# Performance work log

Hardware: AMD Instinct MI355X
Metric: run time of the kernel (lower is better)

Reference implementation:

```python
import jax, jax.numpy as jnp
import numpy as np

B, N, NC = 4, 1024, 512
D, NH, DK, DC = 768, 12, 64, 256
DF = 4 * D
EPS = 1e-5


def _ln(x, g, b):
    m = x.mean(-1, keepdims=True)
    v = ((x - m) ** 2).mean(-1, keepdims=True)
    return (x - m) * jax.lax.rsqrt(v + EPS) * g + b


def setup_inputs() -> dict:
    key = jax.random.key(0)
    ks = jax.random.split(key, 16)
    s = 0.02
    return {
        "x": jax.random.normal(ks[0], (B, N, D), jnp.float32),
        "hdse_bias": jax.random.normal(ks[1], (B, NH, N, N), jnp.float32),
        "context": jax.random.normal(ks[2], (B, NC, DC), jnp.float32),
        "node_mask": jnp.ones((B, N), bool),
        "context_mask": jnp.ones((B, NC), bool),
        "ln_sa_g": jnp.ones((D,), jnp.float32),
        "ln_sa_b": jnp.zeros((D,), jnp.float32),
        "w_qkv": jax.random.normal(ks[3], (D, 3 * D), jnp.float32) * s,
        "b_qkv": jnp.zeros((3 * D,), jnp.float32),
        "w_osa": jax.random.normal(ks[4], (D, D), jnp.float32) * s,
        "b_osa": jnp.zeros((D,), jnp.float32),
        "ln_ca_g": jnp.ones((D,), jnp.float32),
        "ln_ca_b": jnp.zeros((D,), jnp.float32),
        "w_q": jax.random.normal(ks[5], (D, D), jnp.float32) * s,
        "b_q": jnp.zeros((D,), jnp.float32),
        "w_kv": jax.random.normal(ks[6], (DC, 2 * D), jnp.float32) * s,
        "b_kv": jnp.zeros((2 * D,), jnp.float32),
        "w_oca": jax.random.normal(ks[7], (D, D), jnp.float32) * s,
        "b_oca": jnp.zeros((D,), jnp.float32),
        "ln_ff_g": jnp.ones((D,), jnp.float32),
        "ln_ff_b": jnp.zeros((D,), jnp.float32),
        "w_ff1": jax.random.normal(ks[8], (D, DF), jnp.float32) * s,
        "b_ff1": jnp.zeros((DF,), jnp.float32),
        "w_ff2": jax.random.normal(ks[9], (DF, D), jnp.float32) * s,
        "b_ff2": jnp.zeros((D,), jnp.float32),
    }


def reference(x, hdse_bias, context, node_mask, context_mask,
              ln_sa_g, ln_sa_b, w_qkv, b_qkv, w_osa, b_osa,
              ln_ca_g, ln_ca_b, w_q, b_q, w_kv, b_kv, w_oca, b_oca,
              ln_ff_g, ln_ff_b, w_ff1, b_ff1, w_ff2, b_ff2):
    scale = 1.0 / np.sqrt(DK).astype(np.float32)

    # ---- self-attention with HDSE bias ----
    h = _ln(x, ln_sa_g, ln_sa_b)
    qkv = (h @ w_qkv + b_qkv).reshape(B, N, 3, NH, DK)
    q = qkv[:, :, 0].transpose(0, 2, 1, 3)  # (B,NH,N,DK)
    k = qkv[:, :, 1].transpose(0, 2, 1, 3)
    v = qkv[:, :, 2].transpose(0, 2, 1, 3)
    scores = jnp.einsum('bhnd,bhmd->bhnm', q, k) * scale + hdse_bias
    scores = jnp.where(node_mask[:, None, None, :], scores, -1e9)
    attn = jax.nn.softmax(scores, axis=-1)
    sa = jnp.einsum('bhnm,bhmd->bhnd', attn, v).transpose(0, 2, 1, 3).reshape(B, N, D)
    x = x + sa @ w_osa + b_osa

    # ---- cross-attention to context ----
    h = _ln(x, ln_ca_g, ln_ca_b)
    qc = (h @ w_q + b_q).reshape(B, N, NH, DK).transpose(0, 2, 1, 3)
    kvc = (context @ w_kv + b_kv).reshape(B, NC, 2, NH, DK)
    kc = kvc[:, :, 0].transpose(0, 2, 1, 3)  # (B,NH,NC,DK)
    vc = kvc[:, :, 1].transpose(0, 2, 1, 3)
    sc = jnp.einsum('bhnd,bhmd->bhnm', qc, kc) * scale
    sc = jnp.where(context_mask[:, None, None, :], sc, -1e9)
    ca = jnp.einsum('bhnm,bhmd->bhnd', jax.nn.softmax(sc, axis=-1), vc)
    ca = ca.transpose(0, 2, 1, 3).reshape(B, N, D)
    x = x + ca @ w_oca + b_oca

    # ---- FFN (exact GELU, matching nn.GELU default) ----
    h = _ln(x, ln_ff_g, ln_ff_b)
    x = x + jax.nn.gelu(h @ w_ff1 + b_ff1, approximate=False) @ w_ff2 + b_ff2
    return x
```

## Files before the change

kernel.cpp:

```cpp
#include <hip/hip_runtime.h>
#include <hip/hip_bf16.h>
#include <math.h>
#include <stdint.h>

typedef __attribute__((ext_vector_type(8))) short bf16x8;
typedef __attribute__((ext_vector_type(4))) float f32x4;

#define NH_ 12

__global__ __launch_bounds__(256) void wtrans_kernel(const float* __restrict__ W,
    __hip_bfloat16* __restrict__ Wt, int K, int N)
{
  __shared__ float tile[32][33];
  int k0 = blockIdx.x * 32, n0 = blockIdx.y * 32;
  int tx = threadIdx.x & 31, ty = threadIdx.x >> 5;
#pragma unroll
  for (int i = 0; i < 4; i++) {
    int r = ty + i * 8;
    tile[r][tx] = W[(size_t)(k0 + r) * N + n0 + tx];
  }
  __syncthreads();
#pragma unroll
  for (int i = 0; i < 4; i++) {
    int r = ty + i * 8;
    Wt[(size_t)(n0 + r) * K + k0 + tx] = __float2bfloat16(tile[tx][r]);
  }
}

__global__ void cvt_kernel(const float* __restrict__ src, __hip_bfloat16* __restrict__ dst, int n)
{
  int i = blockIdx.x * 256 + threadIdx.x;
  if (i < n) dst[i] = __float2bfloat16(src[i]);
}

__global__ __launch_bounds__(256) void ln_kernel(const float* __restrict__ x,
    const float* __restrict__ gg, const float* __restrict__ bb,
    __hip_bfloat16* __restrict__ out)
{
  int row = blockIdx.x;
  int t = threadIdx.x;
  const float* xr = x + (size_t)row * 768;
  float v0 = xr[t], v1 = xr[t + 256], v2 = xr[t + 512];
  float s = v0 + v1 + v2;
  float s2 = v0 * v0 + v1 * v1 + v2 * v2;
  for (int o = 32; o; o >>= 1) { s += __shfl_down(s, o); s2 += __shfl_down(s2, o); }
  __shared__ float red[8];
  __shared__ float mv[2];
  int wid = t >> 6, lane = t & 63;
  if (lane == 0) { red[wid] = s; red[wid + 4] = s2; }
  __syncthreads();
  if (t == 0) {
    float S = red[0] + red[1] + red[2] + red[3];
    float S2 = red[4] + red[5] + red[6] + red[7];
    float mean = S * (1.0f / 768.0f);
    float var = S2 * (1.0f / 768.0f) - mean * mean;
    mv[0] = mean;
    mv[1] = rsqrtf(var + 1e-5f);
  }
  __syncthreads();
  float mean = mv[0], rstd = mv[1];
  __hip_bfloat16* orow = out + (size_t)row * 768;
  orow[t]       = __float2bfloat16((v0 - mean) * rstd * gg[t] + bb[t]);
  orow[t + 256] = __float2bfloat16((v1 - mean) * rstd * gg[t + 256] + bb[t + 256]);
  orow[t + 512] = __float2bfloat16((v2 - mean) * rstd * gg[t + 512] + bb[t + 512]);
}

__global__ void vtrans_kernel(const __hip_bfloat16* __restrict__ src,
    __hip_bfloat16* __restrict__ dst, int L, int srow, int soff)
{
  int idx = blockIdx.x * 256 + threadIdx.x;
  int n = idx & (L - 1);
  int rest = idx / L;
  int d = rest & 63;
  rest >>= 6;
  int h = rest % NH_;
  int b = rest / NH_;
  dst[idx] = src[(size_t)(b * L + n) * srow + soff + h * 64 + d];
}

template<int EPI>
__global__ __launch_bounds__(256) void gemm_bt(
    const __hip_bfloat16* A, const __hip_bfloat16* Bt,
    const float* __restrict__ bias, const float* resid,
    void* Cout, int M, int N, int K)
{
  __shared__ __align__(16) __hip_bfloat16 As[128 * 32];
  __shared__ __align__(16) __hip_bfloat16 Bs[128 * 32];
  const int tid = threadIdx.x;
  const int bm = blockIdx.y, bn = blockIdx.x;
  const int lane = tid & 63, wid = tid >> 6;
  const int wm = (wid >> 1) * 64, wn = (wid & 1) * 64;
  const int r = lane & 15, g = lane >> 4;
  const int arow = tid >> 2, acol = (tid & 3) * 8;
  f32x4 acc[4][4] = {};
  const __hip_bfloat16* Ag  = A  + (size_t)(bm * 128 + arow) * K + acol;
  const __hip_bfloat16* Ag2 = Ag + (size_t)64 * K;
  const __hip_bfloat16* Bg  = Bt + (size_t)(bn * 128 + arow) * K + acol;
  const __hip_bfloat16* Bg2 = Bg + (size_t)64 * K;
  for (int kt = 0; kt < K; kt += 32) {
    uint4 a0 = *(const uint4*)(Ag + kt);
    uint4 a1 = *(const uint4*)(Ag2 + kt);
    uint4 b0 = *(const uint4*)(Bg + kt);
    uint4 b1 = *(const uint4*)(Bg2 + kt);
    __syncthreads();
    *(uint4*)(As + arow * 32 + acol) = a0;
    *(uint4*)(As + (arow + 64) * 32 + acol) = a1;
    *(uint4*)(Bs + arow * 32 + acol) = b0;
    *(uint4*)(Bs + (arow + 64) * 32 + acol) = b1;
    __syncthreads();
    bf16x8 af[4], bfr[4];
#pragma unroll
    for (int i = 0; i < 4; i++) {
      af[i]  = *(const bf16x8*)(As + (wm + i * 16 + r) * 32 + g * 8);
      bfr[i] = *(const bf16x8*)(Bs + (wn + i * 16 + r) * 32 + g * 8);
    }
#pragma unroll
    for (int i = 0; i < 4; i++)
#pragma unroll
      for (int j = 0; j < 4; j++)
        acc[i][j] = __builtin_amdgcn_mfma_f32_16x16x32_bf16(af[i], bfr[j], acc[i][j], 0, 0, 0);
  }
#pragma unroll
  for (int i = 0; i < 4; i++)
#pragma unroll
    for (int j = 0; j < 4; j++)
#pragma unroll
      for (int q = 0; q < 4; q++) {
        int row = bm * 128 + wm + i * 16 + g * 4 + q;
        int col = bn * 128 + wn + j * 16 + r;
        float v = acc[i][j][q] + bias[col];
        if constexpr (EPI == 0) {
          ((__hip_bfloat16*)Cout)[(size_t)row * N + col] = __float2bfloat16(v);
        } else if constexpr (EPI == 1) {
          ((float*)Cout)[(size_t)row * N + col] = v + resid[(size_t)row * N + col];
        } else {
          float t = 0.5f * v * (1.0f + erff(v * 0.70710678118654752f));
          ((__hip_bfloat16*)Cout)[(size_t)row * N + col] = __float2bfloat16(t);
        }
      }
}

template<int L, bool HASBIAS>
__global__ __launch_bounds__(256) void attn_kernel(
    const __hip_bfloat16* Qp, int qstride,
    const __hip_bfloat16* Kp, int kstride,
    const __hip_bfloat16* Vt,
    const float* __restrict__ bias,
    __hip_bfloat16* Out, float scale)
{
  __shared__ __align__(16) __hip_bfloat16 qtile[16 * 64];
  __shared__ __align__(16) __hip_bfloat16 sP[16 * L];
  __shared__ float invs[16];
  const int qb = blockIdx.x, h = blockIdx.y, b = blockIdx.z;
  const int tid = threadIdx.x, lane = tid & 63, wid = tid >> 6;
  const int r = lane & 15, g = lane >> 4;
  {
    int row = tid >> 4, c4 = (tid & 15) * 4;
    const __hip_bfloat16* src = Qp + (size_t)(b * 1024 + qb * 16 + row) * qstride + h * 64 + c4;
    *(uint2*)(qtile + row * 64 + c4) = *(const uint2*)src;
  }
  __syncthreads();
  bf16x8 q0 = *(const bf16x8*)(qtile + r * 64 + g * 8);
  bf16x8 q1 = *(const bf16x8*)(qtile + r * 64 + 32 + g * 8);
  const int KB = L / 64;
#pragma unroll 4
  for (int kb = 0; kb < KB; kb++) {
    int key0 = wid * (L / 4) + kb * 16;
    const __hip_bfloat16* ks = Kp + (size_t)(b * L + key0 + r) * kstride + h * 64 + g * 8;
    bf16x8 k0 = *(const bf16x8*)ks;
    bf16x8 k1 = *(const bf16x8*)(ks + 32);
    f32x4 acc = {};
    acc = __builtin_amdgcn_mfma_f32_16x16x32_bf16(q0, k0, acc, 0, 0, 0);
    acc = __builtin_amdgcn_mfma_f32_16x16x32_bf16(q1, k1, acc, 0, 0, 0);
    int key = key0 + r;
#pragma unroll
    for (int q = 0; q < 4; q++) {
      int qrow = g * 4 + q;
      float s = acc[q] * scale;
      if constexpr (HASBIAS)
        s += bias[((size_t)(b * NH_ + h) * 1024 + qb * 16 + qrow) * L + key];
      sP[qrow * L + key] = __float2bfloat16(s);
    }
  }
  __syncthreads();
  {
    int row = tid >> 4, j0 = tid & 15;
    float m = -3.0e38f;
    for (int j = j0; j < L; j += 16) m = fmaxf(m, __bfloat162float(sP[row * L + j]));
#pragma unroll
    for (int o = 1; o < 16; o <<= 1) m = fmaxf(m, __shfl_xor(m, o));
    float sum = 0.0f;
    for (int j = j0; j < L; j += 16) {
      float p = expf(__bfloat162float(sP[row * L + j]) - m);
      sum += p;
      sP[row * L + j] = __float2bfloat16(p);
    }
#pragma unroll
    for (int o = 1; o < 16; o <<= 1) sum += __shfl_xor(sum, o);
    if (j0 == 0) invs[row] = 1.0f / sum;
  }
  __syncthreads();
  {
    int d0 = wid * 16;
    const __hip_bfloat16* vs = Vt + ((size_t)(b * NH_ + h) * 64 + d0 + r) * L + g * 8;
    f32x4 acc = {};
    for (int kb = 0; kb < L / 32; kb++) {
      bf16x8 pf = *(const bf16x8*)(sP + r * L + kb * 32 + g * 8);
      bf16x8 vf = *(const bf16x8*)(vs + kb * 32);
      acc = __builtin_amdgcn_mfma_f32_16x16x32_bf16(pf, vf, acc, 0, 0, 0);
    }
#pragma unroll
    for (int q = 0; q < 4; q++) {
      int qrow = g * 4 + q;
      float o = acc[q] * invs[qrow];
      Out[(size_t)(b * 1024 + qb * 16 + qrow) * 768 + h * 64 + d0 + r] = __float2bfloat16(o);
    }
  }
}

extern "C" void kernel_launch(void* const* d_in, const int* in_sizes, int n_in,
                              void* d_out, int out_size, void* d_ws, size_t ws_size,
                              hipStream_t stream)
{
  const float* x       = (const float*)d_in[0];
  const float* hdse    = (const float*)d_in[1];
  const float* ctx     = (const float*)d_in[2];
  const float* ln_sa_g = (const float*)d_in[5];
  const float* ln_sa_b = (const float*)d_in[6];
  const float* w_qkv   = (const float*)d_in[7];
  const float* b_qkv   = (const float*)d_in[8];
  const float* w_osa   = (const float*)d_in[9];
  const float* b_osa   = (const float*)d_in[10];
  const float* ln_ca_g = (const float*)d_in[11];
  const float* ln_ca_b = (const float*)d_in[12];
  const float* w_q     = (const float*)d_in[13];
  const float* b_q     = (const float*)d_in[14];
  const float* w_kv    = (const float*)d_in[15];
  const float* b_kv    = (const float*)d_in[16];
  const float* w_oca   = (const float*)d_in[17];
  const float* b_oca   = (const float*)d_in[18];
  const float* ln_ff_g = (const float*)d_in[19];
  const float* ln_ff_b = (const float*)d_in[20];
  const float* w_ff1   = (const float*)d_in[21];
  const float* b_ff1   = (const float*)d_in[22];
  const float* w_ff2   = (const float*)d_in[23];
  const float* b_ff2   = (const float*)d_in[24];

  char* ws = (char*)d_ws;
  __hip_bfloat16* wqkvT = (__hip_bfloat16*)(ws + 0);
  __hip_bfloat16* wosaT = (__hip_bfloat16*)(ws + 3538944);
  __hip_bfloat16* wqT   = (__hip_bfloat16*)(ws + 4718592);
  __hip_bfloat16* wkvT  = (__hip_bfloat16*)(ws + 5898240);
  __hip_bfloat16* wocaT = (__hip_bfloat16*)(ws + 6684672);
  __hip_bfloat16* wff1T = (__hip_bfloat16*)(ws + 7864320);
  __hip_bfloat16* wff2T = (__hip_bfloat16*)(ws + 12582912);
  __hip_bfloat16* hbf   = (__hip_bfloat16*)(ws + 17301504);
  __hip_bfloat16* qkvb  = (__hip_bfloat16*)(ws + 23592960);
  __hip_bfloat16* vtsa  = (__hip_bfloat16*)(ws + 42467328);
  __hip_bfloat16* ffb   = (__hip_bfloat16*)(ws + 23592960);
  __hip_bfloat16* sab   = (__hip_bfloat16*)(ws + 48758784);
  __hip_bfloat16* cab   = sab;
  __hip_bfloat16* qcb   = (__hip_bfloat16*)(ws + 55050240);
  __hip_bfloat16* ctxb  = (__hip_bfloat16*)(ws + 61341696);
  __hip_bfloat16* kvcb  = (__hip_bfloat16*)(ws + 62390272);
  __hip_bfloat16* vtca  = (__hip_bfloat16*)(ws + 68681728);
  float* xout = (float*)d_out;

  hipLaunchKernelGGL(wtrans_kernel, dim3(24, 72), 256, 0, stream, w_qkv, wqkvT, 768, 2304);
  hipLaunchKernelGGL(wtrans_kernel, dim3(24, 24), 256, 0, stream, w_osa, wosaT, 768, 768);
  hipLaunchKernelGGL(wtrans_kernel, dim3(24, 24), 256, 0, stream, w_q,   wqT,   768, 768);
  hipLaunchKernelGGL(wtrans_kernel, dim3(8, 48),  256, 0, stream, w_kv,  wkvT,  256, 1536);
  hipLaunchKernelGGL(wtrans_kernel, dim3(24, 24), 256, 0, stream, w_oca, wocaT, 768, 768);
  hipLaunchKernelGGL(wtrans_kernel, dim3(24, 96), 256, 0, stream, w_ff1, wff1T, 768, 3072);
  hipLaunchKernelGGL(wtrans_kernel, dim3(96, 24), 256, 0, stream, w_ff2, wff2T, 3072, 768);
  hipLaunchKernelGGL(cvt_kernel, dim3(2048), 256, 0, stream, ctx, ctxb, 2048 * 256);

  hipLaunchKernelGGL(ln_kernel, dim3(4096), 256, 0, stream, x, ln_sa_g, ln_sa_b, hbf);
  hipLaunchKernelGGL((gemm_bt<0>), dim3(18, 32), 256, 0, stream,
                     hbf, wqkvT, b_qkv, (const float*)nullptr, (void*)qkvb, 4096, 2304, 768);
  hipLaunchKernelGGL(vtrans_kernel, dim3(12288), 256, 0, stream, qkvb, vtsa, 1024, 2304, 1536);
  hipLaunchKernelGGL((attn_kernel<1024, true>), dim3(64, 12, 4), 256, 0, stream,
                     qkvb, 2304, qkvb + 768, 2304, vtsa, hdse, sab, 0.125f);
  hipLaunchKernelGGL((gemm_bt<1>), dim3(6, 32), 256, 0, stream,
                     sab, wosaT, b_osa, x, (void*)xout, 4096, 768, 768);

  hipLaunchKernelGGL(ln_kernel, dim3(4096), 256, 0, stream, xout, ln_ca_g, ln_ca_b, hbf);
  hipLaunchKernelGGL((gemm_bt<0>), dim3(6, 32), 256, 0, stream,
                     hbf, wqT, b_q, (const float*)nullptr, (void*)qcb, 4096, 768, 768);
  hipLaunchKernelGGL((gemm_bt<0>), dim3(12, 16), 256, 0, stream,
                     ctxb, wkvT, b_kv, (const float*)nullptr, (void*)kvcb, 2048, 1536, 256);
  hipLaunchKernelGGL(vtrans_kernel, dim3(6144), 256, 0, stream, kvcb, vtca, 512, 1536, 768);
  hipLaunchKernelGGL((attn_kernel<512, false>), dim3(64, 12, 4), 256, 0, stream,
                     qcb, 768, kvcb, 1536, vtca, (const float*)nullptr, cab, 0.125f);
  hipLaunchKernelGGL((gemm_bt<1>), dim3(6, 32), 256, 0, stream,
                     cab, wocaT, b_oca, xout, (void*)xout, 4096, 768, 768);

  hipLaunchKernelGGL(ln_kernel, dim3(4096), 256, 0, stream, xout, ln_ff_g, ln_ff_b, hbf);
  hipLaunchKernelGGL((gemm_bt<2>), dim3(24, 32), 256, 0, stream,
                     hbf, wff1T, b_ff1, (const float*)nullptr, (void*)ffb, 4096, 3072, 768);
  hipLaunchKernelGGL((gemm_bt<1>), dim3(6, 32), 256, 0, stream,
                     ffb, wff2T, b_ff2, xout, (void*)xout, 4096, 768, 3072);
}
```

Baseline: 798.0 us.

## Use direct global-to-LDS loads in GEMM and contiguous K/V layouts for attention

The GEMM tile loads now go straight from global memory into LDS with global_load_lds instead of staging through registers. A new kvprep kernel replaces the scalar V transpose: it uses an LDS tile to build a transposed V and also writes a per-head contiguous K copy, so the attention kernel reads K rows densely. In the attention kernel, the HDSE bias add and scaling move into the softmax pass, where they become vectorized float4 reads, and the score buffer is padded to reduce LDS bank conflicts. The extra K copy adds memory traffic and reuses workspace buffers, which is only safe if those buffers are dead at that point.

```diff
diff --git a/kernel.cpp b/kernel.cpp
--- a/kernel.cpp
+++ b/kernel.cpp
@@ -7,6 +7,12 @@
 typedef __attribute__((ext_vector_type(4))) float f32x4;
 
 #define NH_ 12
+
+typedef __attribute__((address_space(1))) unsigned int as1_uint;
+typedef __attribute__((address_space(3))) unsigned int as3_uint;
+__device__ static inline void gload16(const void* g, void* l) {
+  __builtin_amdgcn_global_load_lds((as1_uint*)g, (as3_uint*)l, 16, 0, 0);
+}
 
 __global__ __launch_bounds__(256) void wtrans_kernel(const float* __restrict__ W,
     __hip_bfloat16* __restrict__ Wt, int K, int N)
@@ -65,17 +71,30 @@
   orow[t + 512] = __float2bfloat16((v2 - mean) * rstd * gg[t + 512] + bb[t + 512]);
 }
 
-__global__ void vtrans_kernel(const __hip_bfloat16* __restrict__ src,
-    __hip_bfloat16* __restrict__ dst, int L, int srow, int soff)
-{
-  int idx = blockIdx.x * 256 + threadIdx.x;
-  int n = idx & (L - 1);
-  int rest = idx / L;
-  int d = rest & 63;
-  rest >>= 6;
-  int h = rest % NH_;
-  int b = rest / NH_;
-  dst[idx] = src[(size_t)(b * L + n) * srow + soff + h * 64 + d];
+__global__ __launch_bounds__(256) void kvprep_kernel(const __hip_bfloat16* __restrict__ src,
+    int srow, int koff, int voff,
+    __hip_bfloat16* __restrict__ Kc, __hip_bfloat16* __restrict__ Vt, int L)
+{
+  __shared__ __align__(16) __hip_bfloat16 t[64][72];
+  int nt = blockIdx.x, h = blockIdx.y, b = blockIdx.z;
+  int rr = threadIdx.x >> 3, c8 = (threadIdx.x & 7) * 8;
+#pragma unroll
+  for (int i = 0; i < 2; i++) {
+    int nloc = rr + i * 32;
+    int n = nt * 64 + nloc;
+    const __hip_bfloat16* s = src + (size_t)(b * L + n) * srow + h * 64;
+    *(uint4*)(Kc + ((size_t)(b * NH_ + h) * L + n) * 64 + c8) = *(const uint4*)(s + koff + c8);
+    *(uint4*)(&t[nloc][c8]) = *(const uint4*)(s + voff + c8);
+  }
+  __syncthreads();
+#pragma unroll
+  for (int i = 0; i < 2; i++) {
+    int d = rr + i * 32;
+    __hip_bfloat16 tmp[8];
+#pragma unroll
+    for (int j = 0; j < 8; j++) tmp[j] = t[c8 + j][d];
+    *(uint4*)(Vt + ((size_t)(b * NH_ + h) * 64 + d) * L + nt * 64 + c8) = *(uint4*)tmp;
+  }
 }
 
 template<int EPI>
@@ -97,16 +116,16 @@
   const __hip_bfloat16* Ag2 = Ag + (size_t)64 * K;
   const __hip_bfloat16* Bg  = Bt + (size_t)(bn * 128 + arow) * K + acol;
   const __hip_bfloat16* Bg2 = Bg + (size_t)64 * K;
+  __hip_bfloat16* lA  = As + tid * 8;
+  __hip_bfloat16* lA2 = As + 64 * 32 + tid * 8;
+  __hip_bfloat16* lB  = Bs + tid * 8;
+  __hip_bfloat16* lB2 = Bs + 64 * 32 + tid * 8;
   for (int kt = 0; kt < K; kt += 32) {
-    uint4 a0 = *(const uint4*)(Ag + kt);
-    uint4 a1 = *(const uint4*)(Ag2 + kt);
-    uint4 b0 = *(const uint4*)(Bg + kt);
-    uint4 b1 = *(const uint4*)(Bg2 + kt);
     __syncthreads();
-    *(uint4*)(As + arow * 32 + acol) = a0;
-    *(uint4*)(As + (arow + 64) * 32 + acol) = a1;
-    *(uint4*)(Bs + arow * 32 + acol) = b0;
-    *(uint4*)(Bs + (arow + 64) * 32 + acol) = b1;
+    gload16(Ag + kt, lA);
+    gload16(Ag2 + kt, lA2);
+    gload16(Bg + kt, lB);
+    gload16(Bg2 + kt, lB2);
     __syncthreads();
     bf16x8 af[4], bfr[4];
 #pragma unroll
@@ -142,14 +161,15 @@
 
 template<int L, bool HASBIAS>
 __global__ __launch_bounds__(256) void attn_kernel(
-    const __hip_bfloat16* Qp, int qstride,
-    const __hip_bfloat16* Kp, int kstride,
-    const __hip_bfloat16* Vt,
+    const __hip_bfloat16* __restrict__ Qp, int qstride,
+    const __hip_bfloat16* __restrict__ Kc,
+    const __hip_bfloat16* __restrict__ Vt,
     const float* __restrict__ bias,
-    __hip_bfloat16* Out, float scale)
-{
+    __hip_bfloat16* __restrict__ Out, float scale)
+{
+  constexpr int SPAD = L + 8;
   __shared__ __align__(16) __hip_bfloat16 qtile[16 * 64];
-  __shared__ __align__(16) __hip_bfloat16 sP[16 * L];
+  __shared__ __align__(16) __hip_bfloat16 sP[16 * SPAD];
   __shared__ float invs[16];
   const int qb = blockIdx.x, h = blockIdx.y, b = blockIdx.z;
   const int tid = threadIdx.x, lane = tid & 63, wid = tid >> 6;
@@ -162,11 +182,11 @@
   __syncthreads();
   bf16x8 q0 = *(const bf16x8*)(qtile + r * 64 + g * 8);
   bf16x8 q1 = *(const bf16x8*)(qtile + r * 64 + 32 + g * 8);
-  const int KB = L / 64;
+  const __hip_bfloat16* kbase = Kc + (size_t)(b * NH_ + h) * L * 64;
 #pragma unroll 4
-  for (int kb = 0; kb < KB; kb++) {
+  for (int kb = 0; kb < L / 64; kb++) {
     int key0 = wid * (L / 4) + kb * 16;
-    const __hip_bfloat16* ks = Kp + (size_t)(b * L + key0 + r) * kstride + h * 64 + g * 8;
+    const __hip_bfloat16* ks = kbase + (key0 + r) * 64 + g * 8;
     bf16x8 k0 = *(const bf16x8*)ks;
     bf16x8 k1 = *(const bf16x8*)(ks + 32);
     f32x4 acc = {};
@@ -174,26 +194,51 @@
     acc = __builtin_amdgcn_mfma_f32_16x16x32_bf16(q1, k1, acc, 0, 0, 0);
     int key = key0 + r;
 #pragma unroll
-    for (int q = 0; q < 4; q++) {
-      int qrow = g * 4 + q;
-      float s = acc[q] * scale;
-      if constexpr (HASBIAS)
-        s += bias[((size_t)(b * NH_ + h) * 1024 + qb * 16 + qrow) * L + key];
-      sP[qrow * L + key] = __float2bfloat16(s);
-    }
+    for (int q = 0; q < 4; q++)
+      sP[(g * 4 + q) * SPAD + key] = __float2bfloat16(acc[q]);
   }
   __syncthreads();
   {
     int row = tid >> 4, j0 = tid & 15;
+    __hip_bfloat16* sprow = sP + row * SPAD;
+    const float* brow = nullptr;
+    if constexpr (HASBIAS)
+      brow = bias + ((size_t)(b * NH_ + h) * 1024 + qb * 16 + row) * L;
     float m = -3.0e38f;
-    for (int j = j0; j < L; j += 16) m = fmaxf(m, __bfloat162float(sP[row * L + j]));
+#pragma unroll
+    for (int it = 0; it < L / 64; it++) {
+      int c = it * 64 + j0 * 4;
+      __hip_bfloat16 t4[4];
+      *(uint2*)t4 = *(uint2*)(sprow + c);
+      float f0 = __bfloat162float(t4[0]) * scale;
+      float f1 = __bfloat162float(t4[1]) * scale;
+      float f2 = __bfloat162float(t4[2]) * scale;
+      float f3 = __bfloat162float(t4[3]) * scale;
+      if constexpr (HASBIAS) {
+        float4 bv = *(const float4*)(brow + c);
+        f0 += bv.x; f1 += bv.y; f2 += bv.z; f3 += bv.w;
+      }
+      m = fmaxf(m, fmaxf(fmaxf(f0, f1), fmaxf(f2, f3)));
+      t4[0] = __float2bfloat16(f0); t4[1] = __float2bfloat16(f1);
+      t4[2] = __float2bfloat16(f2); t4[3] = __float2bfloat16(f3);
+      *(uint2*)(sprow + c) = *(uint2*)t4;
+    }
 #pragma unroll
     for (int o = 1; o < 16; o <<= 1) m = fmaxf(m, __shfl_xor(m, o));
     float sum = 0.0f;
-    for (int j = j0; j < L; j += 16) {
-      float p = expf(__bfloat162float(sP[row * L + j]) - m);
-      sum += p;
-      sP[row * L + j] = __float2bfloat16(p);
+#pragma unroll
+    for (int it = 0; it < L / 64; it++) {
+      int c = it * 64 + j0 * 4;
+      __hip_bfloat16 t4[4];
+      *(uint2*)t4 = *(uint2*)(sprow + c);
+      float e0 = expf(__bfloat162float(t4[0]) - m);
+      float e1 = expf(__bfloat162float(t4[1]) - m);
+      float e2 = expf(__bfloat162float(t4[2]) - m);
+      float e3 = expf(__bfloat162float(t4[3]) - m);
+      sum += (e0 + e1) + (e2 + e3);
+      t4[0] = __float2bfloat16(e0); t4[1] = __float2bfloat16(e1);
+      t4[2] = __float2bfloat16(e2); t4[3] = __float2bfloat16(e3);
+      *(uint2*)(sprow + c) = *(uint2*)t4;
     }
 #pragma unroll
     for (int o = 1; o < 16; o <<= 1) sum += __shfl_xor(sum, o);
@@ -205,7 +250,7 @@
     const __hip_bfloat16* vs = Vt + ((size_t)(b * NH_ + h) * 64 + d0 + r) * L + g * 8;
     f32x4 acc = {};
     for (int kb = 0; kb < L / 32; kb++) {
-      bf16x8 pf = *(const bf16x8*)(sP + r * L + kb * 32 + g * 8);
+      bf16x8 pf = *(const bf16x8*)(sP + r * SPAD + kb * 32 + g * 8);
       bf16x8 vf = *(const bf16x8*)(vs + kb * 32);
       acc = __builtin_amdgcn_mfma_f32_16x16x32_bf16(pf, vf, acc, 0, 0, 0);
     }
@@ -255,7 +300,9 @@
   __hip_bfloat16* wff1T = (__hip_bfloat16*)(ws + 7864320);
   __hip_bfloat16* wff2T = (__hip_bfloat16*)(ws + 12582912);
   __hip_bfloat16* hbf   = (__hip_bfloat16*)(ws + 17301504);
+  __hip_bfloat16* kcsa  = hbf;
   __hip_bfloat16* qkvb  = (__hip_bfloat16*)(ws + 23592960);
+  __hip_bfloat16* kcca  = (__hip_bfloat16*)(ws + 23592960);
   __hip_bfloat16* vtsa  = (__hip_bfloat16*)(ws + 42467328);
   __hip_bfloat16* ffb   = (__hip_bfloat16*)(ws + 23592960);
   __hip_bfloat16* sab   = (__hip_bfloat16*)(ws + 48758784);
@@ -278,9 +325,10 @@
   hipLaunchKernelGGL(ln_kernel, dim3(4096), 256, 0, stream, x, ln_sa_g, ln_sa_b, hbf);
   hipLaunchKernelGGL((gemm_bt<0>), dim3(18, 32), 256, 0, stream,
                      hbf, wqkvT, b_qkv, (const float*)nullptr, (void*)qkvb, 4096, 2304, 768);
-  hipLaunchKernelGGL(vtrans_kernel, dim3(12288), 256, 0, stream, qkvb, vtsa, 1024, 2304, 1536);
+  hipLaunchKernelGGL(kvprep_kernel, dim3(16, 12, 4), 256, 0, stream,
+                     qkvb, 2304, 768, 1536, kcsa, vtsa, 1024);
   hipLaunchKernelGGL((attn_kernel<1024, true>), dim3(64, 12, 4), 256, 0, stream,
-                     qkvb, 2304, qkvb + 768, 2304, vtsa, hdse, sab, 0.125f);
+                     qkvb, 2304, kcsa, vtsa, hdse, sab, 0.125f);
   hipLaunchKernelGGL((gemm_bt<1>), dim3(6, 32), 256, 0, stream,
                      sab, wosaT, b_osa, x, (void*)xout, 4096, 768, 768);
 
@@ -289,9 +337,10 @@
                      hbf, wqT, b_q, (const float*)nullptr, (void*)qcb, 4096, 768, 768);
   hipLaunchKernelGGL((gemm_bt<0>), dim3(12, 16), 256, 0, stream,
                      ctxb, wkvT, b_kv, (const float*)nullptr, (void*)kvcb, 2048, 1536, 256);
-  hipLaunchKernelGGL(vtrans_kernel, dim3(6144), 256, 0, stream, kvcb, vtca, 512, 1536, 768);
+  hipLaunchKernelGGL(kvprep_kernel, dim3(8, 12, 4), 256, 0, stream,
+                     kvcb, 1536, 0, 768, kcca, vtca, 512);
   hipLaunchKernelGGL((attn_kernel<512, false>), dim3(64, 12, 4), 256, 0, stream,
-                     qcb, 768, kvcb, 1536, vtca, (const float*)nullptr, cab, 0.125f);
+                     qcb, 768, kcca, vtca, (const float*)nullptr, cab, 0.125f);
   hipLaunchKernelGGL((gemm_bt<1>), dim3(6, 32), 256, 0, stream,
                      cab, wocaT, b_oca, xout, (void*)xout, 4096, 768, 768);
 
```

New measurement: 762.7 us. 4.4% less time.
